# Kernel tuning notes

Hardware: AMD Instinct MI355X
Metric: run time of the kernel (lower is better)

## Reference

```python
import jax
import jax.numpy as jnp
from jax import lax
import numpy as np

N_COLORS = 256  # n_possible_colors; classifier emits N_COLORS+1 logits (last = 'new color')
LRELU_SLOPE = 0.01  # torch nn.LeakyReLU default negative_slope


def setup_inputs() -> dict:
    key = jax.random.key(0)
    ks = jax.random.split(key, 8)
    N, E = 8192, 512
    deg = 32
    s1 = 1.0 / np.sqrt(2 * E)
    s2 = 1.0 / np.sqrt(E)
    s3 = 1.0 / np.sqrt(400)
    return {
        "embeddings": jax.random.normal(ks[0], (N, E), jnp.float32),
        "neighbors": jax.random.randint(ks[1], (N, deg), 0, N, jnp.int32),
        "W1": jax.random.normal(ks[2], (2 * E, E), jnp.float32) * s1,
        "b1": jnp.zeros((E,), jnp.float32),
        "W2": jax.random.normal(ks[3], (E, 400), jnp.float32) * s2,
        "b2": jnp.zeros((400,), jnp.float32),
        "W3": jax.random.normal(ks[4], (400, N_COLORS + 1), jnp.float32) * s3,
        "b3": jnp.zeros((N_COLORS + 1,), jnp.float32),
        "baseline": jnp.ones((), jnp.float32),
    }


def _leaky(x):
    return jnp.where(x >= 0, x, LRELU_SLOPE * x)


def reference(embeddings, neighbors, W1, b1, W2, b2, W3, b3, baseline):
    N, E = embeddings.shape
    C = N_COLORS + 1  # 257 output classes
    graph_emb = embeddings.mean(axis=0)  # torch.mean(embeddings, dim=0), constant across steps
    idx = jnp.arange(C)
    colors0 = jnp.full((N,), -1, jnp.int32).at[0].set(0)  # _assign_color(0, vertex_order[0])
    key0 = jax.random.key(42)

    def step(carry, v):
        colors, n_used, logp, key = carry
        key, sk = jax.random.split(key)
        # classifier MLP: cat(node_emb, graph_emb) -> 512 -> 400 -> 257
        x = jnp.concatenate([embeddings[v], graph_emb])  # [2E]
        h = _leaky(x @ W1 + b1)
        h = _leaky(h @ W2 + b2)
        logits = h @ W3 + b3  # [257]
        # _mask_irrelevant_colors: disable unused colors in [n_used, 256)
        irrel = (idx >= n_used) & (idx < N_COLORS)
        # _mask_colors: disable colors of already-colored neighbors (-1 = uncolored -> padded out)
        nb_c = colors[neighbors[v]]  # [deg]
        adj_mask = jnp.zeros((C + 1,), bool).at[jnp.where(nb_c < 0, C, nb_c)].set(True)[:C]
        logits = jnp.where(irrel | adj_mask, -jnp.inf, logits)
        probs = jax.nn.softmax(logits)  # classifier output
        raw = jax.random.categorical(sk, logits)  # np.random.choice(p=probs)
        chosen = jnp.where(raw == N_COLORS, n_used, raw).astype(jnp.int32)
        n_used = jnp.where(raw == N_COLORS, n_used + 1, n_used)
        colors = colors.at[v].set(chosen)
        p = probs[raw]
        logp = logp + jnp.log(p + 1e-8) - jnp.log(jnp.asarray(1e-8, p.dtype))
        return (colors, n_used, logp, key), None

    init = (colors0, jnp.int32(1), jnp.float32(0.0), key0)
    (colors, n_used, logp, _), _ = lax.scan(step, init, jnp.arange(1, N))
    loss = (n_used.astype(jnp.float32) - baseline) * logp / N
    return colors, loss
```

## Files before the change

kernel.cpp:

```cpp
#include <hip/hip_runtime.h>
#include <stdint.h>
#include <math.h>

#define NV 8192
#define EMB 512
#define CLS 257
#define DEG 32
#define TV 8
#define RSTRIDE 260

struct KP { uint32_t a, b; };

__host__ __device__ constexpr KP tfc(uint32_t k0, uint32_t k1,
                                     uint32_t x0, uint32_t x1) {
  const uint32_t ks2 = k0 ^ k1 ^ 0x1BD11BDAu;
  uint32_t v0 = x0 + k0, v1 = x1 + k1;
#define QR(r) { v0 += v1; v1 = (v1 << (r)) | (v1 >> (32 - (r))); v1 ^= v0; }
  QR(13) QR(15) QR(26) QR(6)
  v0 += k1;  v1 += ks2 + 1u;
  QR(17) QR(29) QR(16) QR(24)
  v0 += ks2; v1 += k0 + 2u;
  QR(13) QR(15) QR(26) QR(6)
  v0 += k0;  v1 += k1 + 3u;
  QR(17) QR(29) QR(16) QR(24)
  v0 += k1;  v1 += ks2 + 4u;
  QR(13) QR(15) QR(26) QR(6)
  v0 += ks2; v1 += k0 + 5u;
#undef QR
  return KP{v0, v1};
}

struct Seg { KP e[256]; };
constexpr Seg mkseg(KP s) {
  Seg g{};
  g.e[0] = s;
  for (int i = 1; i < 256; ++i) g.e[i] = tfc(g.e[i - 1].a, g.e[i - 1].b, 0u, 0u);
  return g;
}
#define NXTSEG(prev) mkseg(tfc(prev.e[255].a, prev.e[255].b, 0u, 0u))
constexpr Seg SG0 = mkseg(KP{0u, 42u});
constexpr Seg SG1 = NXTSEG(SG0);   constexpr Seg SG2 = NXTSEG(SG1);
constexpr Seg SG3 = NXTSEG(SG2);   constexpr Seg SG4 = NXTSEG(SG3);
constexpr Seg SG5 = NXTSEG(SG4);   constexpr Seg SG6 = NXTSEG(SG5);
constexpr Seg SG7 = NXTSEG(SG6);   constexpr Seg SG8 = NXTSEG(SG7);
constexpr Seg SG9 = NXTSEG(SG8);   constexpr Seg SG10 = NXTSEG(SG9);
constexpr Seg SG11 = NXTSEG(SG10); constexpr Seg SG12 = NXTSEG(SG11);
constexpr Seg SG13 = NXTSEG(SG12); constexpr Seg SG14 = NXTSEG(SG13);
constexpr Seg SG15 = NXTSEG(SG14); constexpr Seg SG16 = NXTSEG(SG15);
constexpr Seg SG17 = NXTSEG(SG16); constexpr Seg SG18 = NXTSEG(SG17);
constexpr Seg SG19 = NXTSEG(SG18); constexpr Seg SG20 = NXTSEG(SG19);
constexpr Seg SG21 = NXTSEG(SG20); constexpr Seg SG22 = NXTSEG(SG21);
constexpr Seg SG23 = NXTSEG(SG22); constexpr Seg SG24 = NXTSEG(SG23);
constexpr Seg SG25 = NXTSEG(SG24); constexpr Seg SG26 = NXTSEG(SG25);
constexpr Seg SG27 = NXTSEG(SG26); constexpr Seg SG28 = NXTSEG(SG27);
constexpr Seg SG29 = NXTSEG(SG28); constexpr Seg SG30 = NXTSEG(SG29);
constexpr Seg SG31 = NXTSEG(SG30);

struct KT { uint32_t hi[8192]; uint32_t lo[8192]; };
constexpr KT mkkt() {
  KT t{};
  const Seg* sg[32] = {
    &SG0,  &SG1,  &SG2,  &SG3,  &SG4,  &SG5,  &SG6,  &SG7,
    &SG8,  &SG9,  &SG10, &SG11, &SG12, &SG13, &SG14, &SG15,
    &SG16, &SG17, &SG18, &SG19, &SG20, &SG21, &SG22, &SG23,
    &SG24, &SG25, &SG26, &SG27, &SG28, &SG29, &SG30, &SG31 };
  for (int s = 0; s < 32; ++s)
    for (int i = 0; i < 256; ++i) {
      const int v = 1 + s * 256 + i;
      if (v < 8192) { t.hi[v] = sg[s]->e[i].a; t.lo[v] = sg[s]->e[i].b; }
    }
  return t;
}
__device__ const KT KEYS = mkkt();

__global__ __launch_bounds__(256) void colmean_part(const float* __restrict__ emb,
                                                    float* __restrict__ part) {
  const int b = blockIdx.x;
  const int t = threadIdx.x;
  for (int j = t; j < EMB; j += 256) {
    float s = 0.f;
    const int r0 = b * 128;
    for (int r = 0; r < 128; ++r) s += emb[(size_t)(r0 + r) * EMB + j];
    part[(size_t)b * EMB + j] = s;
  }
}

__global__ __launch_bounds__(256) void colmean_fin(const float* __restrict__ part,
                                                   float* __restrict__ g) {
  const int t = threadIdx.x;
  for (int j = t; j < EMB; j += 256) {
    float s = 0.f;
    for (int b = 0; b < 64; ++b) s += part[(size_t)b * EMB + j];
    g[j] = s / 8192.0f;
  }
}

__global__ __launch_bounds__(256) void mlp3i(
    const float* __restrict__ emb, const float* __restrict__ g,
    const float* __restrict__ W1, const float* __restrict__ b1,
    const float* __restrict__ W2, const float* __restrict__ b2,
    const float* __restrict__ W3, const float* __restrict__ b3,
    float* __restrict__ pl, float* __restrict__ er)
{
  __shared__ float xs[TV][68];
  __shared__ float gs[EMB];
  __shared__ float h1s[TV][EMB];
  __shared__ float h2s[TV][400];
  __shared__ float redw[TV][4];
  __shared__ float li256s[TV];
  __shared__ float mrs[TV];

  const int t  = threadIdx.x;
  const int v0 = blockIdx.x * TV;
  const int j2 = 2 * t;

  for (int j = t; j < EMB; j += 256) gs[j] = g[j];

  float accA[TV], accB[TV];
#pragma unroll
  for (int vv = 0; vv < TV; ++vv) { accA[vv] = 0.f; accB[vv] = 0.f; }

  for (int kc = 0; kc < 8; ++kc) {
    __syncthreads();
    if (t < 128) {
      const int vv = t >> 4;
      const int kk = (t & 15) << 2;
      const float4 s4 = *reinterpret_cast<const float4*>(
          &emb[(size_t)(v0 + vv) * EMB + kc * 64 + kk]);
      xs[vv][kk] = s4.x; xs[vv][kk + 1] = s4.y;
      xs[vv][kk + 2] = s4.z; xs[vv][kk + 3] = s4.w;
    }
    __syncthreads();
    float cA[TV], cB[TV];
#pragma unroll
    for (int vv = 0; vv < TV; ++vv) { cA[vv] = 0.f; cB[vv] = 0.f; }
    for (int q = 0; q < 16; ++q) {
      const int k = kc * 64 + q * 4;
      float2 w[4];
#pragma unroll
      for (int u = 0; u < 4; ++u)
        w[u] = *reinterpret_cast<const float2*>(&W1[(size_t)(k + u) * EMB + j2]);
      float4 xv[TV];
#pragma unroll
      for (int vv = 0; vv < TV; ++vv)
        xv[vv] = *reinterpret_cast<const float4*>(&xs[vv][q * 4]);
#pragma unroll
      for (int u = 0; u < 4; ++u) {
#pragma unroll
        for (int vv = 0; vv < TV; ++vv) {
          const float x = (u == 0) ? xv[vv].x : (u == 1) ? xv[vv].y
                         : (u == 2) ? xv[vv].z : xv[vv].w;
          cA[vv] = fmaf(x, w[u].x, cA[vv]);
          cB[vv] = fmaf(x, w[u].y, cB[vv]);
        }
      }
    }
#pragma unroll
    for (int vv = 0; vv < TV; ++vv) { accA[vv] += cA[vv]; accB[vv] += cB[vv]; }
  }

  float gA = 0.f, gB = 0.f;
  for (int kc = 0; kc < 8; ++kc) {
    float cgA = 0.f, cgB = 0.f;
    for (int q = 0; q < 16; ++q) {
      const int k = kc * 64 + q * 4;
      const float4 gv = *reinterpret_cast<const float4*>(&gs[k]);
      float2 w[4];
#pragma unroll
      for (int u = 0; u < 4; ++u)
        w[u] = *reinterpret_cast<const float2*>(
            &W1[(size_t)(EMB + k + u) * EMB + j2]);
      cgA = fmaf(gv.x, w[0].x, cgA); cgB = fmaf(gv.x, w[0].y, cgB);
      cgA = fmaf(gv.y, w[1].x, cgA); cgB = fmaf(gv.y, w[1].y, cgB);
      cgA = fmaf(gv.z, w[2].x, cgA); cgB = fmaf(gv.z, w[2].y, cgB);
      cgA = fmaf(gv.w, w[3].x, cgA); cgB = fmaf(gv.w, w[3].y, cgB);
    }
    gA += cgA; gB += cgB;
  }

  {
    const float bA = b1[j2], bB = b1[j2 + 1];
#pragma unroll
    for (int vv = 0; vv < TV; ++vv) {
      float hA = (accA[vv] + gA) + bA;
      float hB = (accB[vv] + gB) + bB;
      hA = (hA >= 0.f) ? hA : 0.01f * hA;
      hB = (hB >= 0.f) ? hB : 0.01f * hB;
      *reinterpret_cast<float2*>(&h1s[vv][j2]) = float2{hA, hB};
    }
  }
  __syncthreads();

  if (t < 200) {
    float a2A[TV], a2B[TV];
#pragma unroll
    for (int vv = 0; vv < TV; ++vv) { a2A[vv] = 0.f; a2B[vv] = 0.f; }
    for (int kc = 0; kc < 8; ++kc) {
      float cA[TV], cB[TV];
#pragma unroll
      for (int vv = 0; vv < TV; ++vv) { cA[vv] = 0.f; cB[vv] = 0.f; }
      for (int q = 0; q < 16; ++q) {
        const int k = kc * 64 + q * 4;
        float2 w[4];
#pragma unroll
        for (int u = 0; u < 4; ++u)
          w[u] = *reinterpret_cast<const float2*>(&W2[(size_t)(k + u) * 400 + j2]);
        float4 hv[TV];
#pragma unroll
        for (int vv = 0; vv < TV; ++vv)
          hv[vv] = *reinterpret_cast<const float4*>(&h1s[vv][k]);
#pragma unroll
        for (int u = 0; u < 4; ++u) {
#pragma unroll
          for (int vv = 0; vv < TV; ++vv) {
            const float x = (u == 0) ? hv[vv].x : (u == 1) ? hv[vv].y
                           : (u == 2) ? hv[vv].z : hv[vv].w;
            cA[vv] = fmaf(x, w[u].x, cA[vv]);
            cB[vv] = fmaf(x, w[u].y, cB[vv]);
          }
        }
      }
#pragma unroll
      for (int vv = 0; vv < TV; ++vv) { a2A[vv] += cA[vv]; a2B[vv] += cB[vv]; }
    }
    const float bA = b2[j2], bB = b2[j2 + 1];
#pragma unroll
    for (int vv = 0; vv < TV; ++vv) {
      float hA = a2A[vv] + bA;
      float hB = a2B[vv] + bB;
      hA = (hA >= 0.f) ? hA : 0.01f * hA;
      hB = (hB >= 0.f) ? hB : 0.01f * hB;
      *reinterpret_cast<float2*>(&h2s[vv][j2]) = float2{hA, hB};
    }
  }
  __syncthreads();

  float a3[TV], a3x[TV];
#pragma unroll
  for (int vv = 0; vv < TV; ++vv) { a3[vv] = 0.f; a3x[vv] = 0.f; }
  for (int kc = 0; kc < 8; ++kc) {
    float c3[TV], c3x[TV];
#pragma unroll
    for (int vv = 0; vv < TV; ++vv) { c3[vv] = 0.f; c3x[vv] = 0.f; }
    for (int kk = 0; kk < 50; ++kk) {
      const int k = kc * 50 + kk;
      const float w0 = W3[(size_t)k * CLS + t];
      const float wx = (t == 0) ? W3[(size_t)k * CLS + 256] : 0.f;
#pragma unroll
      for (int vv = 0; vv < TV; ++vv) {
        const float hv = h2s[vv][k];
        c3[vv]  = fmaf(hv, w0, c3[vv]);
        c3x[vv] = fmaf(hv, wx, c3x[vv]);
      }
    }
#pragma unroll
    for (int vv = 0; vv < TV; ++vv) { a3[vv] += c3[vv]; a3x[vv] += c3x[vv]; }
  }

  const float bj = b3[t];
  float li_[TV];
#pragma unroll
  for (int vv = 0; vv < TV; ++vv) li_[vv] = a3[vv] + bj;

#pragma unroll
  for (int vv = 0; vv < TV; ++vv) {
    float m = li_[vv];
#pragma unroll
    for (int off = 1; off < 64; off <<= 1) m = fmaxf(m, __shfl_xor(m, off));
    if ((t & 63) == 0) redw[vv][t >> 6] = m;
  }
  if (t == 0) {
    const float bx = b3[256];
#pragma unroll
    for (int vv = 0; vv < TV; ++vv) li256s[vv] = a3x[vv] + bx;
  }
  __syncthreads();
  if (t < TV) {
    const float m = fmaxf(fmaxf(redw[t][0], redw[t][1]),
                          fmaxf(redw[t][2], redw[t][3]));
    mrs[t] = fmaxf(m, li256s[t]);
  }
  __syncthreads();

#pragma unroll
  for (int vv = 0; vv < TV; ++vv) {
    const int v = v0 + vv;
    const float li = li_[vv];
    const KP sk = tfc(KEYS.hi[v], KEYS.lo[v], 0u, 1u);
    const KP o  = tfc(sk.a, sk.b, 0u, (uint32_t)t);
    const uint32_t bb = o.a ^ o.b;
    const float f = __uint_as_float(0x3f800000u | (bb >> 9)) - 1.0f;
    const float u = fmaxf(1.17549435e-38f, f);
    const float gg = -logf(-logf(u));
    pl[(size_t)v * RSTRIDE + t] = li + gg;
    er[(size_t)v * RSTRIDE + t] = expf(li - mrs[vv]);
  }
  if (t == 0) {
    const float bx = b3[256];
#pragma unroll
    for (int vv = 0; vv < TV; ++vv) {
      const int v = v0 + vv;
      const float li = a3x[vv] + bx;
      const KP sk = tfc(KEYS.hi[v], KEYS.lo[v], 0u, 1u);
      const KP o  = tfc(sk.a, sk.b, 0u, 256u);
      const uint32_t bb = o.a ^ o.b;
      const float f = __uint_as_float(0x3f800000u | (bb >> 9)) - 1.0f;
      const float u = fmaxf(1.17549435e-38f, f);
      const float gg = -logf(-logf(u));
      pl[(size_t)v * RSTRIDE + 256] = li + gg;
      er[(size_t)v * RSTRIDE + 256] = expf(li - mrs[vv]);
    }
  }
}

#define DPPF(CTRL, OLDI, X) \
  __builtin_amdgcn_update_dpp((int)(OLDI), (X), (CTRL), 0xF, 0xF, false)
#define SRED(CTRL) { S += __int_as_float(DPPF(CTRL, 0, __float_as_int(S))); }

__device__ __forceinline__ uint32_t ordmap(float f) {
  const uint32_t s = __float_as_uint(f);
  return s ^ (0x80000000u | (uint32_t)((int32_t)s >> 31));
}

#define WG_SCOPE __HIP_MEMORY_SCOPE_WORKGROUP

__global__ __launch_bounds__(256) void sortrows(float* __restrict__ plbuf) {
  __shared__ uint64_t keys[4][512];
  const int t = threadIdx.x;
  const int w = t >> 6;
  const int lane = t & 63;
  const int v = blockIdx.x * 4 + w;
  const float* row = plbuf + (size_t)v * RSTRIDE;

#pragma unroll
  for (int j = 0; j < 8; ++j) {
    const int i = lane + 64 * j;
    uint32_t om = 0u;
    if (i < CLS) om = ordmap(row[i]);
    keys[w][i] = ((uint64_t)om << 9) | (uint64_t)(511 - i);
  }
  __syncthreads();

  for (int k = 2; k <= 512; k <<= 1) {
    for (int j = k >> 1; j > 0; j >>= 1) {
#pragma unroll
      for (int m = 0; m < 4; ++m) {
        const int p  = lane + 64 * m;
        const int i  = ((p & ~(j - 1)) << 1) | (p & (j - 1));
        const int ix = i | j;
        const uint64_t a = keys[w][i], b = keys[w][ix];
        const bool sw = ((i & k) == 0) ? (a < b) : (a > b);
        if (sw) { keys[w][i] = b; keys[w][ix] = a; }
      }
      __syncthreads();
    }
  }

  uint16_t* o16 = reinterpret_cast<uint16_t*>(plbuf) + (size_t)v * (RSTRIDE * 2);
#pragma unroll
  for (int j = 0; j < 5; ++j) {
    const int i = lane + 64 * j;
    if (i < 320) o16[i] = (uint16_t)(511u - (uint32_t)(keys[w][i] & 511u));
  }
}

__global__ __launch_bounds__(192) void scan10(
    const int* __restrict__ nbrG, const uint32_t* __restrict__ scG,
    unsigned* __restrict__ rawnu, float* __restrict__ out)
{
  __shared__ int colors[NV];
  __shared__ uint32_t scR[32][160];
  __shared__ int nbrRing[1024];
  __shared__ unsigned bbufW[2][2][16];
  __shared__ int prod_done, consA_done, consB_done;
  __shared__ unsigned relay;

  const int t = threadIdx.x;
  const int wid = t >> 6;
  const int lane = t & 63;
  const int ln32 = lane & 31;
  const uint16_t* scR16 = reinterpret_cast<const uint16_t*>(&scR[0][0]);

  for (int i = t; i < NV; i += 192) colors[i] = -1;
  if (t == 0) {
    colors[0] = 0; prod_done = 0; consA_done = 0; consB_done = 0;
    relay = (0u << 19) | (1u << 9) | 0u;
  }
  __syncthreads();

  if (wid == 2) {
    for (int pc = 0; pc < 1024; ++pc) {
      for (;;) {
        const int ca = __hip_atomic_load(&consA_done, __ATOMIC_ACQUIRE, WG_SCOPE);
        const int cb = __hip_atomic_load(&consB_done, __ATOMIC_ACQUIRE, WG_SCOPE);
        if ((ca < cb ? ca : cb) >= pc - 3) break;
        __builtin_amdgcn_s_sleep(1);
      }
      uint32_t x[8], y[8], z[8];
#pragma unroll
      for (int r = 0; r < 8; ++r) {
        const size_t base = (size_t)(pc * 8 + r) * RSTRIDE;
        x[r] = scG[base + lane];
        y[r] = scG[base + 64 + lane];
        z[r] = (lane < 32) ? scG[base + 128 + lane] : 0u;
      }
      const int4 nb4 = *reinterpret_cast<const int4*>(nbrG + pc * 256 + 4 * lane);
#pragma unroll
      for (int r = 0; r < 8; ++r) {
        const int slot = (pc * 8 + r) & 31;
        scR[slot][lane] = x[r];
        scR[slot][64 + lane] = y[r];
        if (lane < 32) scR[slot][128 + lane] = z[r];
      }
      *reinterpret_cast<int4*>(&nbrRing[((pc & 3) << 8) + 4 * lane]) = nb4;
      if (lane == 0)
        __hip_atomic_store(&prod_done, pc + 1, __ATOMIC_RELEASE, WG_SCOPE);
    }
    return;
  }

  const int v0 = 1 + wid;
  unsigned* const slot0 = bbufW[wid][0];
  unsigned* const slot1 = bbufW[wid][1];

  int pdc = 0;
  while (pdc < 1)
    pdc = __hip_atomic_load(&prod_done, __ATOMIC_ACQUIRE, WG_SCOPE);

  int c0 = 0, c1 = 0;
  bool fb0 = false, fb1 = false, hf = false;

#define PREP10(V) {                                                            \
    const int v_ = (V);                                                        \
    while (pdc <= (v_ >> 3))                                                   \
      pdc = __hip_atomic_load(&prod_done, __ATOMIC_ACQUIRE, WG_SCOPE);         \
    const uint32_t cw_ = scR[v_ & 31][lane];                                   \
    const int nb_ = nbrRing[(((v_ >> 3) & 3) << 8) + ((v_ & 7) << 5) + ln32];  \
    unsigned* const sl_ = ((v_ >> 1) & 1) ? slot1 : slot0;                     \
    sl_[lane & 15] = 0u;                                                       \
    const int cg_ = colors[nb_];                                               \
    hf = (__ballot(nb_ == v_ - 1) != 0ULL);                                    \
    if (cg_ >= 0) atomicOr(&sl_[cg_ >> 5], 1u << (cg_ & 31));                  \
    c0 = (int)(cw_ & 0xFFFFu); c1 = (int)(cw_ >> 16);                          \
    const unsigned w0_ = sl_[c0 >> 5];                                         \
    const unsigned w1_ = sl_[c1 >> 5];                                         \
    fb0 = !((w0_ >> (c0 & 31)) & 1u);                                          \
    fb1 = !((w1_ >> (c1 & 31)) & 1u);                                          \
  }

  PREP10(v0)

  for (int v = v0; v < NV; v += 2) {
    unsigned r;
    do {
      r = __hip_atomic_load(&relay, __ATOMIC_ACQUIRE, WG_SCOPE);
    } while ((r >> 19) != (unsigned)(v - 1));
    const int nu = (int)((r >> 9) & 0x3FFu);
    const int cp = (int)(r & 0x1FFu);

    int raw = 256;
    {
      const bool ok0 = fb0 && (c0 < nu || c0 == 256) && !(hf && c0 == cp);
      const bool ok1 = fb1 && (c1 < nu || c1 == 256) && !(hf && c1 == cp);
      uint64_t b_ = __ballot(ok0 || ok1);
      if (b_) {
        const int sel = ok0 ? c0 : c1;
        raw = __builtin_amdgcn_readlane(sel, (int)__builtin_ctzll(b_));
      } else {
        const int sBv = (v & 31) * 320;
        unsigned* const sl_ = ((v >> 1) & 1) ? slot1 : slot0;
        const int x2 = scR16[sBv + 128 + lane];
        const int x3 = scR16[sBv + 192 + lane];
        const int x4 = scR16[sBv + 256 + lane];
        const unsigned q2 = sl_[x2 >> 5];
        const unsigned q3 = sl_[x3 >> 5];
        const unsigned q4 = sl_[x4 >> 5];
        const bool o2 = (!((q2 >> (x2 & 31)) & 1u)) &&
                        (x2 < nu || x2 == 256) && !(hf && x2 == cp);
        const bool o3 = (!((q3 >> (x3 & 31)) & 1u)) &&
                        (x3 < nu || x3 == 256) && !(hf && x3 == cp);
        const bool o4 = (!((q4 >> (x4 & 31)) & 1u)) &&
                        (x4 < nu || x4 == 256) && !(hf && x4 == cp);
        if ((b_ = __ballot(o2)))
          raw = __builtin_amdgcn_readlane(x2, (int)__builtin_ctzll(b_));
        else if ((b_ = __ballot(o3)))
          raw = __builtin_amdgcn_readlane(x3, (int)__builtin_ctzll(b_));
        else if ((b_ = __ballot(o4)))
          raw = __builtin_amdgcn_readlane(x4, (int)__builtin_ctzll(b_));
      }
    }
    const bool isnew = (raw == 256);
    const int chosen = isnew ? nu : raw;
    const unsigned nuN = (unsigned)nu + (isnew ? 1u : 0u);
    if (lane == 0) {
      colors[v] = chosen;
      rawnu[v] = (unsigned)raw | ((unsigned)nu << 16);
      __hip_atomic_store(&relay,
          ((unsigned)v << 19) | (nuN << 9) | (unsigned)chosen,
          __ATOMIC_RELEASE, WG_SCOPE);
    }

    if ((v & 7) == 7 - wid) {
      const int dn = (v + 1 + wid) >> 3;
      if (lane == 0) {
        if (wid == 0)
          __hip_atomic_store(&consA_done, dn, __ATOMIC_RELEASE, WG_SCOPE);
        else
          __hip_atomic_store(&consB_done, dn, __ATOMIC_RELEASE, WG_SCOPE);
      }
    }

    if (v + 2 < NV) PREP10(v + 2)
  }

  if (lane == 0) {
    if (wid == 0)
      __hip_atomic_store(&consA_done, 1024, __ATOMIC_RELEASE, WG_SCOPE);
    else
      __hip_atomic_store(&consB_done, 1024, __ATOMIC_RELEASE, WG_SCOPE);
  }

  if (wid == 0)
    for (int i = lane; i < NV; i += 64) out[i] = (float)colors[i];
}

__global__ __launch_bounds__(256) void logp_part(
    const float* __restrict__ outF, const int* __restrict__ nbrG,
    const float* __restrict__ er, const unsigned* __restrict__ rawnu,
    double* __restrict__ partd)
{
  __shared__ unsigned bb[4][16];
  const int t = threadIdx.x;
  const int w = t >> 6;
  const int lane = t & 63;
  const int ln32 = lane & 31;
  const int b = blockIdx.x;

  double a = 0.0;
  for (int i = 0; i < 32; ++i) {
    const int v = b * 128 + w * 32 + i;
    if (v == 0) continue;
    const unsigned val = rawnu[v];
    const int raw = (int)(val & 0xFFFFu);
    const int nu  = (int)(val >> 16);

    bb[w][lane & 15] = 0u;
    const int u = nbrG[(size_t)v * DEG + ln32];
    const int cu = (u < v) ? (int)outF[u] : -1;
    if (cu >= 0) atomicOr(&bb[w][cu >> 5], 1u << (cu & 31));
    unsigned bwp[4];
#pragma unroll
    for (int j = 0; j < 4; ++j) bwp[j] = bb[w][(lane >> 5) + 2 * j];
    const unsigned bw8 = bb[w][8];

    const size_t base = (size_t)v * RSTRIDE;
    bool mk[4];
    float e[4];
#pragma unroll
    for (int j = 0; j < 4; ++j) {
      const int c = lane + 64 * j;
      mk[j] = (((bwp[j] >> ln32) & 1u) != 0u) || (c >= nu);
      e[j] = mk[j] ? 0.f : er[base + c];
    }
    const bool mkX = ((bw8 & 1u) != 0u);
    const float eX = er[base + 256];
    const float e4 = (!mkX && lane == 0) ? eX : 0.f;

    float S = ((e[0] + e[1]) + (e[2] + e[3])) + e4;
    SRED(0x111) SRED(0x112) SRED(0x114) SRED(0x118) SRED(0x142) SRED(0x143)
    const float Sall = __int_as_float(
        __builtin_amdgcn_readlane(__float_as_int(S), 63));

    const bool isnew = (raw == 256);
    const int jsel  = isnew ? 4 : (raw >> 6);
    const int owner = isnew ? 0 : (raw & 63);
    const float cand = (jsel == 0) ? e[0] : (jsel == 1) ? e[1]
                     : (jsel == 2) ? e[2] : (jsel == 3) ? e[3] : e4;
    const float praw = __int_as_float(
        __builtin_amdgcn_readlane(__float_as_int(cand), owner));

    const float p = praw / Sall;
    a += (double)(logf(p + 1e-8f) - logf(1e-8f));
  }
  if (lane == 0) partd[b * 4 + w] = a;
}

__global__ __launch_bounds__(64) void finalize(
    const double* __restrict__ partd, const unsigned* __restrict__ rawnu,
    const float* __restrict__ baseline, float* __restrict__ out)
{
  if (threadIdx.x == 0) {
    double lp = 0.0;
    for (int i = 0; i < 256; ++i) lp += partd[i];
    const unsigned val = rawnu[NV - 1];
    const unsigned nf = (val >> 16) + (((val & 0xFFFFu) == 256u) ? 1u : 0u);
    out[NV] = ((float)nf - baseline[0]) * (float)lp / 8192.0f;
  }
}

extern "C" void kernel_launch(void* const* d_in, const int* in_sizes, int n_in,
                              void* d_out, int out_size, void* d_ws, size_t ws_size,
                              hipStream_t stream) {
  const float* emb      = (const float*)d_in[0];
  const int*   nbr      = (const int*)d_in[1];
  const float* W1       = (const float*)d_in[2];
  const float* b1       = (const float*)d_in[3];
  const float* W2       = (const float*)d_in[4];
  const float* b2       = (const float*)d_in[5];
  const float* W3       = (const float*)d_in[6];
  const float* b3       = (const float*)d_in[7];
  const float* baseline = (const float*)d_in[8];
  float* out = (float*)d_out;

  char* ws = (char*)d_ws;
  float* g     = (float*)ws;
  float* plbuf = (float*)(ws + 2048);
  float* erbuf = (float*)(ws + 2048 + NV * RSTRIDE * 4);
  float* part  = erbuf;
  unsigned* rawnu = (unsigned*)(ws + 2048);
  double*   partd = (double*)(ws + 2048 + 65536);

  colmean_part<<<64, 256, 0, stream>>>(emb, part);
  colmean_fin<<<1, 256, 0, stream>>>(part, g);
  mlp3i<<<NV / TV, 256, 0, stream>>>(emb, g, W1, b1, W2, b2, W3, b3, plbuf, erbuf);
  sortrows<<<NV / 4, 256, 0, stream>>>(plbuf);
  scan10<<<1, 192, 0, stream>>>(nbr, (const uint32_t*)plbuf, rawnu, out);
  logp_part<<<64, 256, 0, stream>>>((const float*)out, nbr, erbuf, rawnu, partd);
  finalize<<<1, 64, 0, stream>>>(partd, rawnu, baseline, out);
}
```

Measured before the change: 2.515 ms.

## Software-pipeline scan wave prep further ahead and handle two-back neighbor color

Restructures the serial coloring scan so each wave prefetches its candidate words and neighbor indices two vertices ahead. The neighbor-mask build for the next vertex now overlaps the relay wait and current decision. Because the mask for v+2 is built before v+1 is colored, it adds separate flags for neighbors equal to v+1 (read from the relay) and v (the wave's own last choice). The relay field layout shifts to widen the vertex index and narrow n_used. The aim is to shorten the critical path between consecutive dependent vertices, at the cost of more registers and subtle correctness conditions.

```diff
diff --git a/kernel.cpp b/kernel.cpp
--- a/kernel.cpp
+++ b/kernel.cpp
@@ -364,7 +364,7 @@
   }
 }
 
-__global__ __launch_bounds__(192) void scan10(
+__global__ __launch_bounds__(192) void scan11(
     const int* __restrict__ nbrG, const uint32_t* __restrict__ scG,
     unsigned* __restrict__ rawnu, float* __restrict__ out)
 {
@@ -384,7 +384,7 @@
   for (int i = t; i < NV; i += 192) colors[i] = -1;
   if (t == 0) {
     colors[0] = 0; prod_done = 0; consA_done = 0; consB_done = 0;
-    relay = (0u << 19) | (1u << 9) | 0u;
+    relay = (0u << 18) | (1u << 9) | 0u;
   }
   __syncthreads();
 
@@ -420,67 +420,79 @@
   }
 
   const int v0 = 1 + wid;
-  unsigned* const slot0 = bbufW[wid][0];
-  unsigned* const slot1 = bbufW[wid][1];
+  unsigned* const slotLo = bbufW[wid][0];
+  unsigned* const slotHi = bbufW[wid][1];
 
   int pdc = 0;
   while (pdc < 1)
     pdc = __hip_atomic_load(&prod_done, __ATOMIC_ACQUIRE, WG_SCOPE);
 
-  int c0 = 0, c1 = 0;
-  bool fb0 = false, fb1 = false, hf = false;
-
-#define PREP10(V) {                                                            \
-    const int v_ = (V);                                                        \
-    while (pdc <= (v_ >> 3))                                                   \
-      pdc = __hip_atomic_load(&prod_done, __ATOMIC_ACQUIRE, WG_SCOPE);         \
-    const uint32_t cw_ = scR[v_ & 31][lane];                                   \
-    const int nb_ = nbrRing[(((v_ >> 3) & 3) << 8) + ((v_ & 7) << 5) + ln32];  \
-    unsigned* const sl_ = ((v_ >> 1) & 1) ? slot1 : slot0;                     \
-    sl_[lane & 15] = 0u;                                                       \
-    const int cg_ = colors[nb_];                                               \
-    hf = (__ballot(nb_ == v_ - 1) != 0ULL);                                    \
-    if (cg_ >= 0) atomicOr(&sl_[cg_ >> 5], 1u << (cg_ & 31));                  \
-    c0 = (int)(cw_ & 0xFFFFu); c1 = (int)(cw_ >> 16);                          \
-    const unsigned w0_ = sl_[c0 >> 5];                                         \
-    const unsigned w1_ = sl_[c1 >> 5];                                         \
-    fb0 = !((w0_ >> (c0 & 31)) & 1u);                                          \
-    fb1 = !((w1_ >> (c1 & 31)) & 1u);                                          \
-  }
-
-  PREP10(v0)
+  int c0cur, c1cur;
+  unsigned w0p, w1p;
+  bool f1cur, f2cur;
+  uint32_t cwp;
+  int nbp;
+  int cpOwn = 0;
+  {
+    unsigned* const sl0 = ((v0 >> 1) & 1) ? slotHi : slotLo;
+    sl0[lane & 15] = 0u;
+    const int nb0 = nbrRing[((v0 & 7) << 5) + ln32];
+    const int cg0 = colors[nb0];
+    f1cur = (wid == 1) ? (__ballot(nb0 == 1) != 0ULL) : false;
+    f2cur = false;
+    if (cg0 >= 0) atomicOr(&sl0[cg0 >> 5], 1u << (cg0 & 31));
+    const uint32_t cw0 = scR[v0][lane];
+    c0cur = (int)(cw0 & 0xFFFFu); c1cur = (int)(cw0 >> 16);
+    w0p = sl0[c0cur >> 5];
+    w1p = sl0[c1cur >> 5];
+    cwp = scR[v0 + 2][lane];
+    nbp = nbrRing[(((v0 + 2) & 7) << 5) + ln32];
+  }
 
   for (int v = v0; v < NV; v += 2) {
-    unsigned r;
+    unsigned r_;
     do {
-      r = __hip_atomic_load(&relay, __ATOMIC_ACQUIRE, WG_SCOPE);
-    } while ((r >> 19) != (unsigned)(v - 1));
-    const int nu = (int)((r >> 9) & 0x3FFu);
-    const int cp = (int)(r & 0x1FFu);
+      r_ = __hip_atomic_load(&relay, __ATOMIC_ACQUIRE, WG_SCOPE);
+    } while ((r_ >> 18) != (unsigned)(v - 1));
+    const int nu  = (int)((r_ >> 9) & 0x1FFu);
+    const int cpR = (int)(r_ & 0x1FFu);
+
+    const unsigned w0 = w0p, w1 = w1p;
+    const int c0n = (int)(cwp & 0xFFFFu);
+    const int c1n = (int)(cwp >> 16);
+    const int nbN = nbp;
+
+    unsigned* const slN = (((v + 2) >> 1) & 1) ? slotHi : slotLo;
+    slN[lane & 15] = 0u;
+    const int cgN = colors[nbN];
 
     int raw = 256;
     {
-      const bool ok0 = fb0 && (c0 < nu || c0 == 256) && !(hf && c0 == cp);
-      const bool ok1 = fb1 && (c1 < nu || c1 == 256) && !(hf && c1 == cp);
+      const bool fb0 = !((w0 >> (c0cur & 31)) & 1u);
+      const bool fb1 = !((w1 >> (c1cur & 31)) & 1u);
+      const bool ok0 = fb0 && (c0cur < nu || c0cur == 256)
+                    && !(f1cur && c0cur == cpR) && !(f2cur && c0cur == cpOwn);
+      const bool ok1 = fb1 && (c1cur < nu || c1cur == 256)
+                    && !(f1cur && c1cur == cpR) && !(f2cur && c1cur == cpOwn);
       uint64_t b_ = __ballot(ok0 || ok1);
       if (b_) {
-        const int sel = ok0 ? c0 : c1;
+        const int sel = ok0 ? c0cur : c1cur;
         raw = __builtin_amdgcn_readlane(sel, (int)__builtin_ctzll(b_));
       } else {
+        unsigned* const slV = ((v >> 1) & 1) ? slotHi : slotLo;
         const int sBv = (v & 31) * 320;
-        unsigned* const sl_ = ((v >> 1) & 1) ? slot1 : slot0;
         const int x2 = scR16[sBv + 128 + lane];
         const int x3 = scR16[sBv + 192 + lane];
         const int x4 = scR16[sBv + 256 + lane];
-        const unsigned q2 = sl_[x2 >> 5];
-        const unsigned q3 = sl_[x3 >> 5];
-        const unsigned q4 = sl_[x4 >> 5];
-        const bool o2 = (!((q2 >> (x2 & 31)) & 1u)) &&
-                        (x2 < nu || x2 == 256) && !(hf && x2 == cp);
-        const bool o3 = (!((q3 >> (x3 & 31)) & 1u)) &&
-                        (x3 < nu || x3 == 256) && !(hf && x3 == cp);
-        const bool o4 = (!((q4 >> (x4 & 31)) & 1u)) &&
-                        (x4 < nu || x4 == 256) && !(hf && x4 == cp);
+        const unsigned q2 = slV[x2 >> 5];
+        const unsigned q3 = slV[x3 >> 5];
+        const unsigned q4 = slV[x4 >> 5];
+        const bool o2 = (!((q2 >> (x2 & 31)) & 1u)) && (x2 < nu || x2 == 256)
+                     && !(f1cur && x2 == cpR) && !(f2cur && x2 == cpOwn);
+        const bool o3 = (!((q3 >> (x3 & 31)) & 1u)) && (x3 < nu || x3 == 256)
+                     && !(f1cur && x3 == cpR) && !(f2cur && x3 == cpOwn);
+        const bool o4 = (!((q4 >> (x4 & 31)) & 1u)) && (x4 < nu || x4 == 256)
+                     && !(f1cur && x4 == cpR) && !(f2cur && x4 == cpOwn);
         if ((b_ = __ballot(o2)))
           raw = __builtin_amdgcn_readlane(x2, (int)__builtin_ctzll(b_));
         else if ((b_ = __ballot(o3)))
@@ -491,14 +503,21 @@
     }
     const bool isnew = (raw == 256);
     const int chosen = isnew ? nu : raw;
-    const unsigned nuN = (unsigned)nu + (isnew ? 1u : 0u);
     if (lane == 0) {
       colors[v] = chosen;
       rawnu[v] = (unsigned)raw | ((unsigned)nu << 16);
       __hip_atomic_store(&relay,
-          ((unsigned)v << 19) | (nuN << 9) | (unsigned)chosen,
+          ((unsigned)v << 18) | ((unsigned)(nu + (isnew ? 1 : 0)) << 9)
+            | (unsigned)chosen,
           __ATOMIC_RELEASE, WG_SCOPE);
     }
+    cpOwn = chosen;
+
+    if (cgN >= 0) atomicOr(&slN[cgN >> 5], 1u << (cgN & 31));
+    w0p = slN[c0n >> 5];
+    w1p = slN[c1n >> 5];
+    const bool f1n = (__ballot(nbN == v + 1) != 0ULL);
+    const bool f2n = (__ballot(nbN == v) != 0ULL);
 
     if ((v & 7) == 7 - wid) {
       const int dn = (v + 1 + wid) >> 3;
@@ -510,7 +529,13 @@
       }
     }
 
-    if (v + 2 < NV) PREP10(v + 2)
+    const int r4 = (v + 4 < NV) ? v + 4 : NV - 1;
+    while (pdc <= (r4 >> 3))
+      pdc = __hip_atomic_load(&prod_done, __ATOMIC_ACQUIRE, WG_SCOPE);
+    cwp = scR[r4 & 31][lane];
+    nbp = nbrRing[(((r4 >> 3) & 3) << 8) + ((r4 & 7) << 5) + ln32];
+
+    c0cur = c0n; c1cur = c1n; f1cur = f1n; f2cur = f2n;
   }
 
   if (lane == 0) {
@@ -624,7 +649,7 @@
   colmean_fin<<<1, 256, 0, stream>>>(part, g);
   mlp3i<<<NV / TV, 256, 0, stream>>>(emb, g, W1, b1, W2, b2, W3, b3, plbuf, erbuf);
   sortrows<<<NV / 4, 256, 0, stream>>>(plbuf);
-  scan10<<<1, 192, 0, stream>>>(nbr, (const uint32_t*)plbuf, rawnu, out);
+  scan11<<<1, 192, 0, stream>>>(nbr, (const uint32_t*)plbuf, rawnu, out);
   logp_part<<<64, 256, 0, stream>>>((const float*)out, nbr, erbuf, rawnu, partd);
   finalize<<<1, 64, 0, stream>>>(partd, rawnu, baseline, out);
 }
```

Result: slower. 3.158 ms (+25.6%).

## Process two vertices per relay handoff in the sequential coloring scan

Applied to the files above, without the earlier changes.

The serial scan kernel now has each consumer wave resolve a pair of consecutive vertices per turn instead of one. The two waves alternate on pairs. The relay carries the last two chosen colors and the color count, and intra-pair dependencies (vertex B adjacent to A, or either adjacent to the previous two) are handled through explicit banned-color comparisons. This halves the number of cross-wave acquire/release handoffs on the serial critical path, at the cost of more per-step work and a longer dependency chain inside each wave. The final color writeback moves to the other wave.

```diff
diff --git a/kernel.cpp b/kernel.cpp
--- a/kernel.cpp
+++ b/kernel.cpp
@@ -364,16 +364,75 @@
   }
 }
 
-__global__ __launch_bounds__(192) void scan10(
+#define CRIT12(ROW, C0, C1, W0, W1, NUV, BX, BY, BZ, SLPTR, RAWV) {            \
+    const bool ok0_ = (!((W0 >> (C0 & 31)) & 1u)) && (C0 < NUV || C0 == 256)   \
+                   && C0 != BX && C0 != BY && C0 != BZ;                        \
+    const bool ok1_ = (!((W1 >> (C1 & 31)) & 1u)) && (C1 < NUV || C1 == 256)   \
+                   && C1 != BX && C1 != BY && C1 != BZ;                        \
+    uint64_t b_ = __ballot(ok0_ || ok1_);                                      \
+    if (b_) {                                                                  \
+      const int sel_ = ok0_ ? C0 : C1;                                         \
+      RAWV = __builtin_amdgcn_readlane(sel_, (int)__builtin_ctzll(b_));        \
+    } else {                                                                   \
+      const int sB_ = ((ROW) & 31) * 320;                                      \
+      const int x2_ = scR16[sB_ + 128 + lane];                                 \
+      const int x3_ = scR16[sB_ + 192 + lane];                                 \
+      const int x4_ = scR16[sB_ + 256 + lane];                                 \
+      const unsigned q2_ = SLPTR[x2_ >> 5];                                    \
+      const unsigned q3_ = SLPTR[x3_ >> 5];                                    \
+      const unsigned q4_ = SLPTR[x4_ >> 5];                                    \
+      const bool o2_ = (!((q2_ >> (x2_ & 31)) & 1u)) && (x2_ < NUV || x2_ == 256) \
+                    && x2_ != BX && x2_ != BY && x2_ != BZ;                    \
+      const bool o3_ = (!((q3_ >> (x3_ & 31)) & 1u)) && (x3_ < NUV || x3_ == 256) \
+                    && x3_ != BX && x3_ != BY && x3_ != BZ;                    \
+      const bool o4_ = (!((q4_ >> (x4_ & 31)) & 1u)) && (x4_ < NUV || x4_ == 256) \
+                    && x4_ != BX && x4_ != BY && x4_ != BZ;                    \
+      if ((b_ = __ballot(o2_)))                                                \
+        RAWV = __builtin_amdgcn_readlane(x2_, (int)__builtin_ctzll(b_));       \
+      else if ((b_ = __ballot(o3_)))                                           \
+        RAWV = __builtin_amdgcn_readlane(x3_, (int)__builtin_ctzll(b_));       \
+      else if ((b_ = __ballot(o4_)))                                           \
+        RAWV = __builtin_amdgcn_readlane(x4_, (int)__builtin_ctzll(b_));       \
+    }                                                                          \
+  }
+
+#define PREP12(RA, PAR) {                                                      \
+    const int ra_ = (RA);                                                      \
+    const int rb_ = (ra_ + 1 < NV) ? ra_ + 1 : NV - 1;                         \
+    while (pdc <= (rb_ >> 3))                                                  \
+      pdc = __hip_atomic_load(&prod_done, __ATOMIC_ACQUIRE, WG_SCOPE);         \
+    const uint32_t cwA_ = scR[ra_ & 31][lane];                                 \
+    const uint32_t cwB_ = scR[rb_ & 31][lane];                                 \
+    const int nbA_ = nbrRing[(((ra_ >> 3) & 3) << 8) + ((ra_ & 7) << 5) + ln32]; \
+    const int nbB_ = nbrRing[(((rb_ >> 3) & 3) << 8) + ((rb_ & 7) << 5) + ln32]; \
+    unsigned* const slA_ = bbufW[wid][PAR][0];                                 \
+    unsigned* const slB_ = bbufW[wid][PAR][1];                                 \
+    slA_[lane & 15] = 0u; slB_[lane & 15] = 0u;                                \
+    const int cga_ = colors[nbA_];                                             \
+    const int cgb_ = colors[nbB_];                                             \
+    aF1 = (__ballot(nbA_ == ra_ - 1) != 0ULL);                                 \
+    aF2 = (__ballot(nbA_ == ra_ - 2) != 0ULL);                                 \
+    bFo = (__ballot(nbB_ == ra_) != 0ULL);                                     \
+    bF1 = (__ballot(nbB_ == ra_ - 1) != 0ULL);                                 \
+    bF2 = (__ballot(nbB_ == ra_ - 2) != 0ULL);                                 \
+    if (cga_ >= 0) atomicOr(&slA_[cga_ >> 5], 1u << (cga_ & 31));              \
+    if (cgb_ >= 0) atomicOr(&slB_[cgb_ >> 5], 1u << (cgb_ & 31));              \
+    cA0 = (int)(cwA_ & 0xFFFFu); cA1 = (int)(cwA_ >> 16);                      \
+    cB0 = (int)(cwB_ & 0xFFFFu); cB1 = (int)(cwB_ >> 16);                      \
+    wA0 = slA_[cA0 >> 5]; wA1 = slA_[cA1 >> 5];                                \
+    wB0 = slB_[cB0 >> 5]; wB1 = slB_[cB1 >> 5];                                \
+  }
+
+__global__ __launch_bounds__(192) void scan12(
     const int* __restrict__ nbrG, const uint32_t* __restrict__ scG,
     unsigned* __restrict__ rawnu, float* __restrict__ out)
 {
   __shared__ int colors[NV];
   __shared__ uint32_t scR[32][160];
   __shared__ int nbrRing[1024];
-  __shared__ unsigned bbufW[2][2][16];
+  __shared__ unsigned bbufW[2][2][2][16];
   __shared__ int prod_done, consA_done, consB_done;
-  __shared__ unsigned relay;
+  __shared__ unsigned relayW[2];
 
   const int t = threadIdx.x;
   const int wid = t >> 6;
@@ -384,7 +443,8 @@
   for (int i = t; i < NV; i += 192) colors[i] = -1;
   if (t == 0) {
     colors[0] = 0; prod_done = 0; consA_done = 0; consB_done = 0;
-    relay = (0u << 19) | (1u << 9) | 0u;
+    relayW[0] = 0u;
+    relayW[1] = (0u << 10) | 1u;
   }
   __syncthreads();
 
@@ -419,98 +479,71 @@
     return;
   }
 
-  const int v0 = 1 + wid;
-  unsigned* const slot0 = bbufW[wid][0];
-  unsigned* const slot1 = bbufW[wid][1];
-
   int pdc = 0;
   while (pdc < 1)
     pdc = __hip_atomic_load(&prod_done, __ATOMIC_ACQUIRE, WG_SCOPE);
 
-  int c0 = 0, c1 = 0;
-  bool fb0 = false, fb1 = false, hf = false;
-
-#define PREP10(V) {                                                            \
-    const int v_ = (V);                                                        \
-    while (pdc <= (v_ >> 3))                                                   \
-      pdc = __hip_atomic_load(&prod_done, __ATOMIC_ACQUIRE, WG_SCOPE);         \
-    const uint32_t cw_ = scR[v_ & 31][lane];                                   \
-    const int nb_ = nbrRing[(((v_ >> 3) & 3) << 8) + ((v_ & 7) << 5) + ln32];  \
-    unsigned* const sl_ = ((v_ >> 1) & 1) ? slot1 : slot0;                     \
-    sl_[lane & 15] = 0u;                                                       \
-    const int cg_ = colors[nb_];                                               \
-    hf = (__ballot(nb_ == v_ - 1) != 0ULL);                                    \
-    if (cg_ >= 0) atomicOr(&sl_[cg_ >> 5], 1u << (cg_ & 31));                  \
-    c0 = (int)(cw_ & 0xFFFFu); c1 = (int)(cw_ >> 16);                          \
-    const unsigned w0_ = sl_[c0 >> 5];                                         \
-    const unsigned w1_ = sl_[c1 >> 5];                                         \
-    fb0 = !((w0_ >> (c0 & 31)) & 1u);                                          \
-    fb1 = !((w1_ >> (c1 & 31)) & 1u);                                          \
-  }
-
-  PREP10(v0)
-
-  for (int v = v0; v < NV; v += 2) {
-    unsigned r;
+  int cA0, cA1, cB0, cB1;
+  unsigned wA0, wA1, wB0, wB1;
+  bool aF1, aF2, bFo, bF1, bF2;
+
+  int va = 1 + 2 * wid;
+  PREP12(va, (va >> 2) & 1)
+  if (wid == 0) { aF1 = false; aF2 = false; bF1 = false; bF2 = false; }
+
+  for (; va < NV; va += 4) {
+    const bool hasB = (va + 1 < NV);
+    const int vb = hasB ? va + 1 : va;
+
+    unsigned w1_;
     do {
-      r = __hip_atomic_load(&relay, __ATOMIC_ACQUIRE, WG_SCOPE);
-    } while ((r >> 19) != (unsigned)(v - 1));
-    const int nu = (int)((r >> 9) & 0x3FFu);
-    const int cp = (int)(r & 0x1FFu);
-
-    int raw = 256;
-    {
-      const bool ok0 = fb0 && (c0 < nu || c0 == 256) && !(hf && c0 == cp);
-      const bool ok1 = fb1 && (c1 < nu || c1 == 256) && !(hf && c1 == cp);
-      uint64_t b_ = __ballot(ok0 || ok1);
-      if (b_) {
-        const int sel = ok0 ? c0 : c1;
-        raw = __builtin_amdgcn_readlane(sel, (int)__builtin_ctzll(b_));
-      } else {
-        const int sBv = (v & 31) * 320;
-        unsigned* const sl_ = ((v >> 1) & 1) ? slot1 : slot0;
-        const int x2 = scR16[sBv + 128 + lane];
-        const int x3 = scR16[sBv + 192 + lane];
-        const int x4 = scR16[sBv + 256 + lane];
-        const unsigned q2 = sl_[x2 >> 5];
-        const unsigned q3 = sl_[x3 >> 5];
-        const unsigned q4 = sl_[x4 >> 5];
-        const bool o2 = (!((q2 >> (x2 & 31)) & 1u)) &&
-                        (x2 < nu || x2 == 256) && !(hf && x2 == cp);
-        const bool o3 = (!((q3 >> (x3 & 31)) & 1u)) &&
-                        (x3 < nu || x3 == 256) && !(hf && x3 == cp);
-        const bool o4 = (!((q4 >> (x4 & 31)) & 1u)) &&
-                        (x4 < nu || x4 == 256) && !(hf && x4 == cp);
-        if ((b_ = __ballot(o2)))
-          raw = __builtin_amdgcn_readlane(x2, (int)__builtin_ctzll(b_));
-        else if ((b_ = __ballot(o3)))
-          raw = __builtin_amdgcn_readlane(x3, (int)__builtin_ctzll(b_));
-        else if ((b_ = __ballot(o4)))
-          raw = __builtin_amdgcn_readlane(x4, (int)__builtin_ctzll(b_));
-      }
-    }
-    const bool isnew = (raw == 256);
-    const int chosen = isnew ? nu : raw;
-    const unsigned nuN = (unsigned)nu + (isnew ? 1u : 0u);
+      w1_ = __hip_atomic_load(&relayW[1], __ATOMIC_ACQUIRE, WG_SCOPE);
+    } while ((int)(w1_ >> 10) != va - 1);
+    const unsigned w0_ = relayW[0];
+    const int nu   = (int)(w1_ & 0x3FFu);
+    const int cpP1 = (int)(w0_ & 0x1FFu);
+    const int cpP2 = (int)((w0_ >> 9) & 0x1FFu);
+
+    unsigned* const slA = bbufW[wid][(va >> 2) & 1][0];
+    unsigned* const slB = bbufW[wid][(va >> 2) & 1][1];
+
+    const int BA1 = aF1 ? cpP2 : 511;
+    const int BA2 = aF2 ? cpP1 : 511;
+    int rawA = 256;
+    CRIT12(va, cA0, cA1, wA0, wA1, nu, BA1, BA2, 511, slA, rawA)
+    const bool newA = (rawA == 256);
+    const int chosenA = newA ? nu : rawA;
+    const int nu1 = nu + (newA ? 1 : 0);
+
+    int rawB = 256, chosenB = chosenA, nu2 = nu1;
+    if (hasB) {
+      const int BB0 = bFo ? chosenA : 511;
+      const int BB1 = bF1 ? cpP2 : 511;
+      const int BB2 = bF2 ? cpP1 : 511;
+      CRIT12(vb, cB0, cB1, wB0, wB1, nu1, BB0, BB1, BB2, slB, rawB)
+      const bool newB = (rawB == 256);
+      chosenB = newB ? nu1 : rawB;
+      nu2 = nu1 + (newB ? 1 : 0);
+    }
+
     if (lane == 0) {
-      colors[v] = chosen;
-      rawnu[v] = (unsigned)raw | ((unsigned)nu << 16);
-      __hip_atomic_store(&relay,
-          ((unsigned)v << 19) | (nuN << 9) | (unsigned)chosen,
-          __ATOMIC_RELEASE, WG_SCOPE);
-    }
-
-    if ((v & 7) == 7 - wid) {
-      const int dn = (v + 1 + wid) >> 3;
-      if (lane == 0) {
-        if (wid == 0)
-          __hip_atomic_store(&consA_done, dn, __ATOMIC_RELEASE, WG_SCOPE);
-        else
-          __hip_atomic_store(&consB_done, dn, __ATOMIC_RELEASE, WG_SCOPE);
-      }
-    }
-
-    if (v + 2 < NV) PREP10(v + 2)
+      colors[va] = chosenA;
+      rawnu[va] = (unsigned)rawA | ((unsigned)nu << 16);
+      if (hasB) {
+        colors[vb] = chosenB;
+        rawnu[vb] = (unsigned)rawB | ((unsigned)nu1 << 16);
+      }
+      relayW[0] = (unsigned)chosenA | ((unsigned)chosenB << 9);
+      __hip_atomic_store(&relayW[1],
+          ((unsigned)vb << 10) | (unsigned)nu2, __ATOMIC_RELEASE, WG_SCOPE);
+      const int dn = (vb + 1) >> 3;
+      if (wid == 0)
+        __hip_atomic_store(&consA_done, dn, __ATOMIC_RELEASE, WG_SCOPE);
+      else
+        __hip_atomic_store(&consB_done, dn, __ATOMIC_RELEASE, WG_SCOPE);
+    }
+
+    if (va + 4 < NV) PREP12(va + 4, ((va + 4) >> 2) & 1)
   }
 
   if (lane == 0) {
@@ -520,7 +553,7 @@
       __hip_atomic_store(&consB_done, 1024, __ATOMIC_RELEASE, WG_SCOPE);
   }
 
-  if (wid == 0)
+  if (wid == 1)
     for (int i = lane; i < NV; i += 64) out[i] = (float)colors[i];
 }
 
@@ -624,7 +657,7 @@
   colmean_fin<<<1, 256, 0, stream>>>(part, g);
   mlp3i<<<NV / TV, 256, 0, stream>>>(emb, g, W1, b1, W2, b2, W3, b3, plbuf, erbuf);
   sortrows<<<NV / 4, 256, 0, stream>>>(plbuf);
-  scan10<<<1, 192, 0, stream>>>(nbr, (const uint32_t*)plbuf, rawnu, out);
+  scan12<<<1, 192, 0, stream>>>(nbr, (const uint32_t*)plbuf, rawnu, out);
   logp_part<<<64, 256, 0, stream>>>((const float*)out, nbr, erbuf, rawnu, partd);
   finalize<<<1, 64, 0, stream>>>(partd, rawnu, baseline, out);
 }
```

Result: slower. 2.964 ms (+17.8%).
